# Performance work log

Hardware: AMD Instinct MI355X
Metric: run time of the kernel (lower is better)

Reference implementation:

```python
import jax, jax.numpy as jnp
import numpy as np

DIM = 1536
HEADS = 12
HD = DIM // HEADS           # 128
C = HD // 2                 # 64 rotary pairs per head
B = 1
F_, H_, W_ = 16, 16, 16
S = F_ * H_ * W_            # 4096
MAXPOS = 1024
EPS = 1e-6
SPLITS = (C - 2 * (C // 3), C // 3, C // 3)  # (22, 21, 21)


def setup_inputs() -> dict:
    key = jax.random.key(0)
    ks = jax.random.split(key, 8)
    std = 0.02
    x = jax.random.normal(ks[0], (B, S, DIM), jnp.float32)
    seq_lens = jnp.full((B,), S, dtype=jnp.int32)
    grid_sizes = jnp.tile(jnp.array([[F_, H_, W_]], jnp.int32), (B, 1))
    # rotary angle table: per split, theta_j = pos / 10000^(j/size)
    angs = []
    pos = jnp.arange(MAXPOS, dtype=jnp.float32)
    for sz in SPLITS:
        inv = 1.0 / (10000.0 ** (jnp.arange(sz, dtype=jnp.float32) / sz))
        angs.append(jnp.outer(pos, inv))
    freqs = jnp.concatenate(angs, axis=1)  # [MAXPOS, C]
    return {
        "x": x,
        "seq_lens": seq_lens,
        "grid_sizes": grid_sizes,
        "freqs": freqs,
        "wq": jax.random.normal(ks[1], (DIM, DIM), jnp.float32) * std,
        "bq": jnp.zeros((DIM,), jnp.float32),
        "wk": jax.random.normal(ks[2], (DIM, DIM), jnp.float32) * std,
        "bk": jnp.zeros((DIM,), jnp.float32),
        "wv": jax.random.normal(ks[3], (DIM, DIM), jnp.float32) * std,
        "bv": jnp.zeros((DIM,), jnp.float32),
        "wo": jax.random.normal(ks[4], (DIM, DIM), jnp.float32) * std,
        "bo": jnp.zeros((DIM,), jnp.float32),
        "gq": jnp.ones((DIM,), jnp.float32),
        "gk": jnp.ones((DIM,), jnp.float32),
    }


def _rms_norm(x, g):
    # x * rsqrt(mean(x^2) + eps) * g  (WanRMSNorm)
    var = jnp.mean(jnp.square(x), axis=-1, keepdims=True)
    return x * jax.lax.rsqrt(var + EPS) * g


def _rope(x, freqs, f, h, w):
    # x: [b, s, n, hd]; freqs: [MAXPOS, C] angles; grid (f,h,w), s = f*h*w
    fa = freqs[:f, : SPLITS[0]]
    ha = freqs[:h, SPLITS[0] : SPLITS[0] + SPLITS[1]]
    wa = freqs[:w, SPLITS[0] + SPLITS[1] :]
    ang = jnp.concatenate(
        [
            jnp.broadcast_to(fa[:, None, None, :], (f, h, w, SPLITS[0])),
            jnp.broadcast_to(ha[None, :, None, :], (f, h, w, SPLITS[1])),
            jnp.broadcast_to(wa[None, None, :, :], (f, h, w, SPLITS[2])),
        ],
        axis=-1,
    ).reshape(f * h * w, 1, C)  # [s, 1, C] broadcasts over heads
    cos, sin = jnp.cos(ang), jnp.sin(ang)
    xr = x[..., 0::2]  # real parts of complex pairs
    xi = x[..., 1::2]  # imag parts
    out_r = xr * cos - xi * sin
    out_i = xr * sin + xi * cos
    return jnp.stack([out_r, out_i], axis=-1).reshape(x.shape)


def reference(x, seq_lens, grid_sizes, freqs, wq, bq, wk, bk, wv, bv, wo, bo, gq, gk):
    b, s = x.shape[:2]
    q = _rms_norm(x @ wq.T + bq, gq).reshape(b, s, HEADS, HD)
    k = _rms_norm(x @ wk.T + bk, gk).reshape(b, s, HEADS, HD)
    v = (x @ wv.T + bv).reshape(b, s, HEADS, HD)
    # all samples share the same grid (static for jit)
    q = _rope(q, freqs, F_, H_, W_)
    k = _rope(k, freqs, F_, H_, W_)
    scale = 1.0 / np.sqrt(HD)
    scores = jnp.einsum("bqnd,bknd->bnqk", q, k) * scale  # [b, n, s, s]
    k_pos = jnp.arange(s)
    mask = k_pos[None, None, None, :] < seq_lens[:, None, None, None]
    scores = scores + jnp.where(mask, 0.0, -1e9)
    attn = jax.nn.softmax(scores, axis=-1)
    out = jnp.einsum("bnqk,bknd->bqnd", attn, v).reshape(b, s, DIM)
    return out @ wo.T + bo
```

## Files before the change

kernel.cpp:

```cpp
#include <hip/hip_runtime.h>
#include <hip/hip_bf16.h>

#define DIM   1536
#define HEADS 12
#define HD    128
#define SEQ   4096
#define QSCALE 0.08838834764831845f
#define LOG2E 1.44269504088896f

typedef __attribute__((ext_vector_type(8))) short short8;
typedef __attribute__((ext_vector_type(4))) float f32x4;
typedef __attribute__((ext_vector_type(16))) float f32x16;

__device__ __forceinline__ unsigned short f2bf(float f) {
    __hip_bfloat16 h = __float2bfloat16(f);
    return *reinterpret_cast<unsigned short*>(&h);
}
__device__ __forceinline__ float bf2f(unsigned short u) {
    return __uint_as_float(((unsigned int)u) << 16);
}
__device__ __forceinline__ void async_cp16(void* lds, const void* g) {
    __builtin_amdgcn_global_load_lds(
        (const __attribute__((address_space(1))) unsigned int*)g,
        (__attribute__((address_space(3))) unsigned int*)lds, 16, 0, 0);
}

__global__ __launch_bounds__(256) void convert_bf16(
    const float* __restrict__ src, __hip_bfloat16* __restrict__ dst, int n8)
{
    const int i = blockIdx.x * 256 + threadIdx.x;
    if (i >= n8) return;
    const float4 a = *reinterpret_cast<const float4*>(src + (size_t)i * 8);
    const float4 b = *reinterpret_cast<const float4*>(src + (size_t)i * 8 + 4);
    uint4 o;
    o.x = (unsigned int)f2bf(a.x) | ((unsigned int)f2bf(a.y) << 16);
    o.y = (unsigned int)f2bf(a.z) | ((unsigned int)f2bf(a.w) << 16);
    o.z = (unsigned int)f2bf(b.x) | ((unsigned int)f2bf(b.y) << 16);
    o.w = (unsigned int)f2bf(b.z) | ((unsigned int)f2bf(b.w) << 16);
    *reinterpret_cast<uint4*>(dst + (size_t)i * 8) = o;
}

__global__ __launch_bounds__(256) void convert_all(
    const float* __restrict__ x,  const float* __restrict__ wq,
    const float* __restrict__ wk, const float* __restrict__ wv,
    __hip_bfloat16* __restrict__ xb,  __hip_bfloat16* __restrict__ wqb,
    __hip_bfloat16* __restrict__ wkb, __hip_bfloat16* __restrict__ wvb)
{
    const int i = blockIdx.x * 256 + threadIdx.x;
    const float* src;
    __hip_bfloat16* dst;
    int off;
    if (i < 786432)            { src = x;  dst = xb;  off = i; }
    else if (i < 1081344)      { src = wq; dst = wqb; off = i - 786432; }
    else if (i < 1376256)      { src = wk; dst = wkb; off = i - 1081344; }
    else                       { src = wv; dst = wvb; off = i - 1376256; }
    const float4 a = *reinterpret_cast<const float4*>(src + (size_t)off * 8);
    const float4 b = *reinterpret_cast<const float4*>(src + (size_t)off * 8 + 4);
    uint4 o;
    o.x = (unsigned int)f2bf(a.x) | ((unsigned int)f2bf(a.y) << 16);
    o.y = (unsigned int)f2bf(a.z) | ((unsigned int)f2bf(a.w) << 16);
    o.z = (unsigned int)f2bf(b.x) | ((unsigned int)f2bf(b.y) << 16);
    o.w = (unsigned int)f2bf(b.z) | ((unsigned int)f2bf(b.w) << 16);
    *reinterpret_cast<uint4*>(dst + (size_t)off * 8) = o;
}

__global__ __launch_bounds__(256) void gemm_qkv(
    const __hip_bfloat16* __restrict__ xb,
    const __hip_bfloat16* __restrict__ wqb, const float* __restrict__ bq,
    const __hip_bfloat16* __restrict__ wkb, const float* __restrict__ bk,
    const __hip_bfloat16* __restrict__ wvb, const float* __restrict__ bv,
    __hip_bfloat16* __restrict__ yq, __hip_bfloat16* __restrict__ yk,
    __hip_bfloat16* __restrict__ vrow)
{
    __shared__ __align__(16) short As[128][32];
    __shared__ __align__(16) short Bs[128][32];
    const int z  = blockIdx.z;
    const __hip_bfloat16* W = (z == 0) ? wqb : (z == 1) ? wkb : wvb;
    const float* bias = (z == 0) ? bq : (z == 1) ? bk : bv;
    __hip_bfloat16* outp = (z == 0) ? yq : (z == 1) ? yk : vrow;
    const int bm0 = blockIdx.x * 128;
    const int bn0 = blockIdx.y * 128;
    const int tid  = threadIdx.x;
    const int lane = tid & 63;
    const int wid  = tid >> 6;
    const int wm = (wid >> 1) * 64;
    const int wn = (wid & 1)  * 64;
    const int fr = lane & 15;
    const int fc = (lane >> 4) * 8;
    const int srow = tid >> 2;
    const int scol = (tid & 3) * 8;

    f32x4 acc[4][4] = {};

    for (int kt = 0; kt < DIM; kt += 32) {
        #pragma unroll
        for (int i = 0; i < 2; i++) {
            async_cp16(&As[i * 64 + (wid << 4)][0],
                       xb + (size_t)(bm0 + i * 64 + srow) * DIM + kt + scol);
            async_cp16(&Bs[i * 64 + (wid << 4)][0],
                       W + (size_t)(bn0 + i * 64 + srow) * DIM + kt + scol);
        }
        __syncthreads();
        short8 af[4], bf8[4];
        #pragma unroll
        for (int m = 0; m < 4; m++) af[m]  = *reinterpret_cast<const short8*>(&As[wm + m * 16 + fr][fc]);
        #pragma unroll
        for (int n = 0; n < 4; n++) bf8[n] = *reinterpret_cast<const short8*>(&Bs[wn + n * 16 + fr][fc]);
        #pragma unroll
        for (int m = 0; m < 4; m++)
            #pragma unroll
            for (int n = 0; n < 4; n++)
                acc[m][n] = __builtin_amdgcn_mfma_f32_16x16x32_bf16(af[m], bf8[n], acc[m][n], 0, 0, 0);
        __syncthreads();
    }

    const int crow0 = bm0 + wm + (lane >> 4) * 4;
    const int ccol0 = bn0 + wn + fr;
    #pragma unroll
    for (int n = 0; n < 4; n++) {
        const int col = ccol0 + n * 16;
        const float bb = bias[col];
        #pragma unroll
        for (int m = 0; m < 4; m++)
            #pragma unroll
            for (int r = 0; r < 4; r++)
                outp[(size_t)(crow0 + m * 16 + r) * DIM + col] =
                    __float2bfloat16(acc[m][n][r] + bb);
    }
}

__global__ __launch_bounds__(256) void norm_rope_transpose(
    __hip_bfloat16* __restrict__ yq, __hip_bfloat16* __restrict__ yk,
    const float* __restrict__ gq, const float* __restrict__ gk,
    const float* __restrict__ freqs,
    const __hip_bfloat16* __restrict__ vrow, __hip_bfloat16* __restrict__ vT)
{
    __shared__ float red[4];
    __shared__ __align__(16) short tile[64][72];
    const int b = blockIdx.x;
    const int t = threadIdx.x;

    if (b < 8192) {
        const int s = b >> 1;
        const int z = b & 1;
        __hip_bfloat16* y = z ? yk : yq;
        const float* g = z ? gk : gq;

        float xr[3], xi[3];
        float ss = 0.f;
        #pragma unroll
        for (int i = 0; i < 3; i++) {
            const int p = t + i * 256;
            const unsigned int uu = *reinterpret_cast<const unsigned int*>(&y[(size_t)s * DIM + 2 * p]);
            xr[i] = bf2f((unsigned short)(uu & 0xffffu));
            xi[i] = bf2f((unsigned short)(uu >> 16));
            ss += xr[i] * xr[i] + xi[i] * xi[i];
        }
        #pragma unroll
        for (int m = 1; m < 64; m <<= 1) ss += __shfl_xor(ss, m, 64);
        if ((t & 63) == 0) red[t >> 6] = ss;
        __syncthreads();
        const float sum = red[0] + red[1] + red[2] + red[3];
        const float rs = rsqrtf(sum * (1.0f / DIM) + 1e-6f);
        const int f = s >> 8, hh = (s >> 4) & 15, ww = s & 15;
        const float osc = z ? 1.0f : QSCALE;
        #pragma unroll
        for (int i = 0; i < 3; i++) {
            const int p = t + i * 256;
            const int cc = p & 63;
            const int pos = (cc < 22) ? f : (cc < 43) ? hh : ww;
            const float ang = freqs[pos * 64 + cc];
            float sn, cs;
            sincosf(ang, &sn, &cs);
            const float a = xr[i] * rs * g[2 * p];
            const float bb = xi[i] * rs * g[2 * p + 1];
            const unsigned int pk = (unsigned int)f2bf((a * cs - bb * sn) * osc)
                                  | ((unsigned int)f2bf((a * sn + bb * cs) * osc) << 16);
            *reinterpret_cast<unsigned int*>(&y[(size_t)s * DIM + 2 * p]) = pk;
        }
    } else {
        const int tb = b - 8192;
        const int s0 = (tb & 63) * 64;
        const int c0 = (tb >> 6) * 64;
        #pragma unroll
        for (int i = 0; i < 2; i++) {
            const int ch = t + i * 256;
            const int r = ch >> 3, cc = (ch & 7) * 8;
            *reinterpret_cast<int4*>(&tile[r][cc]) =
                *reinterpret_cast<const int4*>(&vrow[(size_t)(s0 + r) * DIM + c0 + cc]);
        }
        __syncthreads();
        #pragma unroll
        for (int i = 0; i < 2; i++) {
            const int ch = t + i * 256;
            const int c = ch & 63, sc = (ch >> 6) * 8;
            unsigned int w0 = (unsigned short)tile[sc + 0][c] | ((unsigned int)(unsigned short)tile[sc + 1][c] << 16);
            unsigned int w1 = (unsigned short)tile[sc + 2][c] | ((unsigned int)(unsigned short)tile[sc + 3][c] << 16);
            unsigned int w2 = (unsigned short)tile[sc + 4][c] | ((unsigned int)(unsigned short)tile[sc + 5][c] << 16);
            unsigned int w3 = (unsigned short)tile[sc + 6][c] | ((unsigned int)(unsigned short)tile[sc + 7][c] << 16);
            int4 val;
            val.x = (int)w0; val.y = (int)w1; val.z = (int)w2; val.w = (int)w3;
            *reinterpret_cast<int4*>(&vT[(size_t)(c0 + c) * SEQ + s0 + sc]) = val;
        }
    }
}

__global__ __launch_bounds__(256, 2) void flash_attn(
    const __hip_bfloat16* __restrict__ qb,
    const __hip_bfloat16* __restrict__ kb,
    const __hip_bfloat16* __restrict__ vT,
    const int* __restrict__ seq_lens,
    __hip_bfloat16* __restrict__ attno)
{
    __shared__ __align__(16) short Ks[2][64][128];
    __shared__ __align__(16) short Vs[3][128][64];
    const int qt = blockIdx.x;
    const int h  = blockIdx.y;
    const int tid = threadIdx.x;
    const int lane = tid & 63;
    const int w = tid >> 6;
    const int q5 = lane & 31;
    const int hi = lane >> 5;
    const int seqlen = seq_lens[0];
    const int swz = (lane & 7) << 4;
    const int NT = SEQ / 64;

    short8 qf[8];
    const int qrow = qt * 128 + w * 32 + q5;
    #pragma unroll
    for (int s = 0; s < 8; s++)
        qf[s] = *reinterpret_cast<const short8*>(&qb[(size_t)qrow * DIM + h * HD + s * 16 + hi * 8]);

    f32x16 oacc[4] = {};
    float m = -1e30f, l = 0.f;
    unsigned int WpG[4][4];

    const int kROW = w * 4 + (lane >> 4);
    const int kCOL = ((lane & 15) ^ (kROW & 7)) * 8;
    const int vROW = w * 8 + (lane >> 3);
    const int vCOL = (((lane & 7) ^ (vROW & 7))) * 8;

    auto stageK = [&](int tile, int slot) {
        #pragma unroll
        for (int i = 0; i < 4; i++)
            async_cp16(&Ks[slot][i * 16 + w * 4][0],
                       kb + (size_t)(tile * 64 + i * 16 + kROW) * DIM + h * HD + kCOL);
    };
    auto stageV = [&](int tile, int slot) {
        #pragma unroll
        for (int i = 0; i < 4; i++)
            async_cp16(&Vs[slot][i * 32 + vROW][0],
                       vT + ((size_t)h * HD + i * 32 + vROW) * SEQ + tile * 64 + vCOL);
    };
    auto pv = [&](int slot) {
        const char* Vp = (const char*)&Vs[slot][0][0];
        __builtin_amdgcn_s_setprio(1);
        #pragma unroll
        for (int ks = 0; ks < 4; ks++) {
            int4 pwv;
            pwv.x = (int)WpG[ks][0];
            pwv.y = (int)WpG[ks][1];
            pwv.z = (int)WpG[ks][2];
            pwv.w = (int)WpG[ks][3];
            const short8 pf = __builtin_bit_cast(short8, pwv);
            #pragma unroll
            for (int cb = 0; cb < 4; cb++) {
                short8 vf = *reinterpret_cast<const short8*>(
                    Vp + (cb * 32 + q5) * 128 + ((ks * 32 + hi * 16) ^ swz));
                oacc[cb] = __builtin_amdgcn_mfma_f32_32x32x16_bf16(vf, pf, oacc[cb], 0, 0, 0);
            }
        }
        __builtin_amdgcn_s_setprio(0);
    };
    auto softmax_pack = [&](int tt, f32x16* S) {
        const int kbase = tt * 64;
        float v[32];
        if (kbase + 64 <= seqlen) {
            #pragma unroll
            for (int kbk = 0; kbk < 2; kbk++)
                #pragma unroll
                for (int r = 0; r < 16; r++) v[kbk * 16 + r] = S[kbk][r];
        } else {
            #pragma unroll
            for (int kbk = 0; kbk < 2; kbk++)
                #pragma unroll
                for (int r = 0; r < 16; r++) {
                    const int key = kbase + kbk * 32 + (r & 3) + 8 * (r >> 2) + 4 * hi;
                    const float sv = (key < seqlen) ? S[kbk][r] : -1e30f;
                    S[kbk][r] = sv;
                    v[kbk * 16 + r] = sv;
                }
        }
        #pragma unroll
        for (int st = 16; st >= 1; st >>= 1)
            #pragma unroll
            for (int i = 0; i < st; i++) v[i] = fmaxf(v[i], v[i + st]);
        float tmax = fmaxf(v[0], __shfl_xor(v[0], 32, 64));

        if (!__all(tmax <= m + 8.0f)) {
            const float mn = fmaxf(m, tmax);
            const float alpha = exp2f((m - mn) * LOG2E);
            m = mn;
            l *= alpha;
            #pragma unroll
            for (int cb = 0; cb < 4; cb++)
                #pragma unroll
                for (int r = 0; r < 16; r++) oacc[cb][r] *= alpha;
        }
        const float nmL = -m * LOG2E;
        #pragma unroll
        for (int kbk = 0; kbk < 2; kbk++)
            #pragma unroll
            for (int r = 0; r < 16; r++) {
                const float p = exp2f(fmaf(S[kbk][r], LOG2E, nmL));
                S[kbk][r] = p;
                v[kbk * 16 + r] = p;
            }
        #pragma unroll
        for (int st = 16; st >= 1; st >>= 1)
            #pragma unroll
            for (int i = 0; i < st; i++) v[i] += v[i + st];
        l += v[0] + __shfl_xor(v[0], 32, 64);

        unsigned int Wl[2][4][2];
        #pragma unroll
        for (int kbk = 0; kbk < 2; kbk++)
            #pragma unroll
            for (int tq = 0; tq < 4; tq++) {
                Wl[kbk][tq][0] = (unsigned int)f2bf(S[kbk][4 * tq + 0])
                               | ((unsigned int)f2bf(S[kbk][4 * tq + 1]) << 16);
                Wl[kbk][tq][1] = (unsigned int)f2bf(S[kbk][4 * tq + 2])
                               | ((unsigned int)f2bf(S[kbk][4 * tq + 3]) << 16);
            }
        #pragma unroll
        for (int ks = 0; ks < 4; ks++) {
            const int kbk = ks >> 1;
            const int te = (ks & 1) * 2, to = te + 1;
            const int a0 = (int)Wl[kbk][te][0], a1 = (int)Wl[kbk][te][1];
            const int b0 = (int)Wl[kbk][to][0], b1 = (int)Wl[kbk][to][1];
            const int xa0 = __shfl_xor(a0, 32, 64);
            const int xa1 = __shfl_xor(a1, 32, 64);
            const int xb0 = __shfl_xor(b0, 32, 64);
            const int xb1 = __shfl_xor(b1, 32, 64);
            WpG[ks][0] = (unsigned int)(hi ? xb0 : a0);
            WpG[ks][1] = (unsigned int)(hi ? xb1 : a1);
            WpG[ks][2] = (unsigned int)(hi ? b0  : xa0);
            WpG[ks][3] = (unsigned int)(hi ? b1  : xa1);
        }
    };
    auto qk = [&](int slot, f32x16* S) {
        const char* Kp = (const char*)&Ks[slot][0][0];
        __builtin_amdgcn_s_setprio(1);
        #pragma unroll
        for (int s = 0; s < 8; s++)
            #pragma unroll
            for (int kbk = 0; kbk < 2; kbk++) {
                short8 kf = *reinterpret_cast<const short8*>(
                    Kp + (kbk * 32 + q5) * 256 + ((s * 32 + hi * 16) ^ swz));
                S[kbk] = __builtin_amdgcn_mfma_f32_32x32x16_bf16(kf, qf[s], S[kbk], 0, 0, 0);
            }
        __builtin_amdgcn_s_setprio(0);
    };

    stageK(0, 0); stageV(0, 0);
    __syncthreads();
    stageK(1, 1); stageV(1, 1);
    {
        f32x16 sacc[2] = {};
        qk(0, sacc);
        softmax_pack(0, sacc);
    }

    int vprev = 0, vnext = 2;
    for (int t = 1; t < NT; t++) {
        __syncthreads();
        if (t + 1 < NT) {
            stageK(t + 1, (t + 1) & 1);
            stageV(t + 1, vnext);
        }
        f32x16 sacc[2] = {};
        qk(t & 1, sacc);
        pv(vprev);
        softmax_pack(t, sacc);
        vprev = (vprev == 2) ? 0 : vprev + 1;
        vnext = (vnext == 2) ? 0 : vnext + 1;
    }

    pv(vprev);

    const float inv_l = 1.f / l;
    const size_t obase = (size_t)qrow * DIM + h * HD;
    #pragma unroll
    for (int cb = 0; cb < 4; cb++) {
        #pragma unroll
        for (int tq = 0; tq < 4; tq++) {
            uint2 pko;
            pko.x = (unsigned int)f2bf(oacc[cb][4 * tq + 0] * inv_l)
                  | ((unsigned int)f2bf(oacc[cb][4 * tq + 1] * inv_l) << 16);
            pko.y = (unsigned int)f2bf(oacc[cb][4 * tq + 2] * inv_l)
                  | ((unsigned int)f2bf(oacc[cb][4 * tq + 3] * inv_l) << 16);
            *reinterpret_cast<uint2*>(&attno[obase + cb * 32 + 8 * tq + 4 * hi]) = pko;
        }
    }
}

__global__ __launch_bounds__(256) void gemm_out(
    const __hip_bfloat16* __restrict__ A,
    const __hip_bfloat16* __restrict__ W,
    const float* __restrict__ bias,
    float* __restrict__ outp)
{
    __shared__ __align__(16) short As[128][32];
    __shared__ __align__(16) short Bs[128][32];
    const int bm0 = blockIdx.x * 128;
    const int bn0 = blockIdx.y * 128;
    const int tid = threadIdx.x;
    const int lane = tid & 63;
    const int wid = tid >> 6;
    const int wm = (wid >> 1) * 64;
    const int wn = (wid & 1) * 64;
    const int fr = lane & 15;
    const int fc = (lane >> 4) * 8;
    const int srow = tid >> 2;
    const int scol = (tid & 3) * 8;

    f32x4 acc[4][4] = {};

    for (int kt = 0; kt < DIM; kt += 32) {
        #pragma unroll
        for (int i = 0; i < 2; i++) {
            async_cp16(&As[i * 64 + (wid << 4)][0],
                       A + (size_t)(bm0 + i * 64 + srow) * DIM + kt + scol);
            async_cp16(&Bs[i * 64 + (wid << 4)][0],
                       W + (size_t)(bn0 + i * 64 + srow) * DIM + kt + scol);
        }
        __syncthreads();
        short8 af[4], bf8[4];
        #pragma unroll
        for (int m = 0; m < 4; m++) af[m]  = *reinterpret_cast<const short8*>(&As[wm + m * 16 + fr][fc]);
        #pragma unroll
        for (int n = 0; n < 4; n++) bf8[n] = *reinterpret_cast<const short8*>(&Bs[wn + n * 16 + fr][fc]);
        #pragma unroll
        for (int m = 0; m < 4; m++)
            #pragma unroll
            for (int n = 0; n < 4; n++)
                acc[m][n] = __builtin_amdgcn_mfma_f32_16x16x32_bf16(af[m], bf8[n], acc[m][n], 0, 0, 0);
        __syncthreads();
    }

    const int crow0 = bm0 + wm + (lane >> 4) * 4;
    const int ccol0 = bn0 + wn + fr;
    #pragma unroll
    for (int n = 0; n < 4; n++) {
        const int col = ccol0 + n * 16;
        const float bb = bias[col];
        #pragma unroll
        for (int m = 0; m < 4; m++)
            #pragma unroll
            for (int r = 0; r < 4; r++)
                outp[(size_t)(crow0 + m * 16 + r) * DIM + col] = acc[m][n][r] + bb;
    }
}

extern "C" void kernel_launch(void* const* d_in, const int* in_sizes, int n_in,
                              void* d_out, int out_size, void* d_ws, size_t ws_size,
                              hipStream_t stream)
{
    const float* x        = (const float*)d_in[0];
    const int*   seq_lens = (const int*)d_in[1];
    const float* freqs    = (const float*)d_in[3];
    const float* wq = (const float*)d_in[4];
    const float* bq = (const float*)d_in[5];
    const float* wk = (const float*)d_in[6];
    const float* bk = (const float*)d_in[7];
    const float* wv = (const float*)d_in[8];
    const float* bv = (const float*)d_in[9];
    const float* wo = (const float*)d_in[10];
    const float* bo = (const float*)d_in[11];
    const float* gq = (const float*)d_in[12];
    const float* gk = (const float*)d_in[13];
    float* out = (float*)d_out;

    char* ws = (char*)d_ws;
    __hip_bfloat16* yq    = (__hip_bfloat16*)(ws);
    __hip_bfloat16* yk    = (__hip_bfloat16*)(ws + 12582912);
    __hip_bfloat16* vrow  = (__hip_bfloat16*)(ws + 25165824);
    __hip_bfloat16* vT    = (__hip_bfloat16*)(ws + 37748736);
    __hip_bfloat16* attno = (__hip_bfloat16*)(ws + 25165824);
    __hip_bfloat16* xb    = (__hip_bfloat16*)(ws + 37748736);
    __hip_bfloat16* wob   = (__hip_bfloat16*)(ws);
    __hip_bfloat16* wqb   = (__hip_bfloat16*)d_out;
    __hip_bfloat16* wkb   = wqb + 2359296;
    __hip_bfloat16* wvb   = wkb + 2359296;

    dim3 blk(256);
    convert_all        <<<dim3(6528), blk, 0, stream>>>(x, wq, wk, wv, xb, wqb, wkb, wvb);
    gemm_qkv           <<<dim3(32, 12, 3), blk, 0, stream>>>(xb, wqb, bq, wkb, bk, wvb, bv, yq, yk, vrow);
    norm_rope_transpose<<<dim3(9728), blk, 0, stream>>>(yq, yk, gq, gk, freqs, vrow, vT);
    flash_attn         <<<dim3(32, 12), blk, 0, stream>>>(yq, yk, vT, seq_lens, attno);
    convert_bf16       <<<dim3(1152), blk, 0, stream>>>(wo, wob, 294912);
    gemm_out           <<<dim3(32, 12), blk, 0, stream>>>(attno, wob, bo, out);
}
```

Before: 323.3 us.

## Process two 32-row query tiles per wave in flash attention with 128-thread blocks

Result: slower. 406.3 us (+25.7%).

```diff
diff --git a/kernel.cpp b/kernel.cpp
--- a/kernel.cpp
+++ b/kernel.cpp
@@ -205,7 +205,7 @@
     }
 }
 
-__global__ __launch_bounds__(256, 2) void flash_attn(
+__global__ __launch_bounds__(128, 1) void flash_attn(
     const __hip_bfloat16* __restrict__ qb,
     const __hip_bfloat16* __restrict__ kb,
     const __hip_bfloat16* __restrict__ vT,
@@ -225,71 +225,90 @@
     const int swz = (lane & 7) << 4;
     const int NT = SEQ / 64;
 
-    short8 qf[8];
-    const int qrow = qt * 128 + w * 32 + q5;
+    const int qrowA = qt * 128 + w * 64 + q5;
+    const int qrowB = qrowA + 32;
+    short8 qfA[8], qfB[8];
     #pragma unroll
-    for (int s = 0; s < 8; s++)
-        qf[s] = *reinterpret_cast<const short8*>(&qb[(size_t)qrow * DIM + h * HD + s * 16 + hi * 8]);
-
-    f32x16 oacc[4] = {};
-    float m = -1e30f, l = 0.f;
-    unsigned int WpG[4][4];
-
-    const int kROW = w * 4 + (lane >> 4);
-    const int kCOL = ((lane & 15) ^ (kROW & 7)) * 8;
-    const int vROW = w * 8 + (lane >> 3);
-    const int vCOL = (((lane & 7) ^ (vROW & 7))) * 8;
+    for (int s = 0; s < 8; s++) {
+        qfA[s] = *reinterpret_cast<const short8*>(&qb[(size_t)qrowA * DIM + h * HD + s * 16 + hi * 8]);
+        qfB[s] = *reinterpret_cast<const short8*>(&qb[(size_t)qrowB * DIM + h * HD + s * 16 + hi * 8]);
+    }
+
+    f32x16 oaccA[4] = {}, oaccB[4] = {};
+    float mA = -1e30f, lA = 0.f, mB = -1e30f, lB = 0.f;
+    unsigned int WpGA[4][4], WpGB[4][4];
+
+    const int kROW0 = w * 4 + (lane >> 4);
+    const int kCOL  = ((lane & 15) ^ kROW0) * 8;
+    const int vROW0 = w * 8 + (lane >> 3);
+    const int vCOL  = ((lane & 7) ^ (vROW0 & 7)) * 8;
 
     auto stageK = [&](int tile, int slot) {
         #pragma unroll
-        for (int i = 0; i < 4; i++)
-            async_cp16(&Ks[slot][i * 16 + w * 4][0],
-                       kb + (size_t)(tile * 64 + i * 16 + kROW) * DIM + h * HD + kCOL);
+        for (int i = 0; i < 8; i++)
+            async_cp16(&Ks[slot][i * 8 + w * 4][0],
+                       kb + (size_t)(tile * 64 + i * 8 + kROW0) * DIM + h * HD + kCOL);
     };
     auto stageV = [&](int tile, int slot) {
         #pragma unroll
-        for (int i = 0; i < 4; i++)
-            async_cp16(&Vs[slot][i * 32 + vROW][0],
-                       vT + ((size_t)h * HD + i * 32 + vROW) * SEQ + tile * 64 + vCOL);
+        for (int i = 0; i < 8; i++)
+            async_cp16(&Vs[slot][i * 16 + vROW0][0],
+                       vT + ((size_t)h * HD + i * 16 + vROW0) * SEQ + tile * 64 + vCOL);
+    };
+    auto qk = [&](int slot, f32x16* SA, f32x16* SB) {
+        const char* Kp = (const char*)&Ks[slot][0][0];
+        __builtin_amdgcn_s_setprio(1);
+        #pragma unroll
+        for (int s = 0; s < 8; s++) {
+            #pragma unroll
+            for (int kbk = 0; kbk < 2; kbk++) {
+                short8 kf = *reinterpret_cast<const short8*>(
+                    Kp + (kbk * 32 + q5) * 256 + ((s * 32 + hi * 16) ^ swz));
+                SA[kbk] = __builtin_amdgcn_mfma_f32_32x32x16_bf16(kf, qfA[s], SA[kbk], 0, 0, 0);
+                SB[kbk] = __builtin_amdgcn_mfma_f32_32x32x16_bf16(kf, qfB[s], SB[kbk], 0, 0, 0);
+            }
+        }
+        __builtin_amdgcn_s_setprio(0);
     };
     auto pv = [&](int slot) {
         const char* Vp = (const char*)&Vs[slot][0][0];
         __builtin_amdgcn_s_setprio(1);
         #pragma unroll
         for (int ks = 0; ks < 4; ks++) {
-            int4 pwv;
-            pwv.x = (int)WpG[ks][0];
-            pwv.y = (int)WpG[ks][1];
-            pwv.z = (int)WpG[ks][2];
-            pwv.w = (int)WpG[ks][3];
-            const short8 pf = __builtin_bit_cast(short8, pwv);
+            int4 pa, pb;
+            pa.x = (int)WpGA[ks][0]; pa.y = (int)WpGA[ks][1];
+            pa.z = (int)WpGA[ks][2]; pa.w = (int)WpGA[ks][3];
+            pb.x = (int)WpGB[ks][0]; pb.y = (int)WpGB[ks][1];
+            pb.z = (int)WpGB[ks][2]; pb.w = (int)WpGB[ks][3];
+            const short8 pfA = __builtin_bit_cast(short8, pa);
+            const short8 pfB = __builtin_bit_cast(short8, pb);
             #pragma unroll
             for (int cb = 0; cb < 4; cb++) {
                 short8 vf = *reinterpret_cast<const short8*>(
                     Vp + (cb * 32 + q5) * 128 + ((ks * 32 + hi * 16) ^ swz));
-                oacc[cb] = __builtin_amdgcn_mfma_f32_32x32x16_bf16(vf, pf, oacc[cb], 0, 0, 0);
+                oaccA[cb] = __builtin_amdgcn_mfma_f32_32x32x16_bf16(vf, pfA, oaccA[cb], 0, 0, 0);
+                oaccB[cb] = __builtin_amdgcn_mfma_f32_32x32x16_bf16(vf, pfB, oaccB[cb], 0, 0, 0);
             }
         }
         __builtin_amdgcn_s_setprio(0);
     };
-    auto softmax_pack = [&](int tt, f32x16* S) {
+    auto softmax_pack = [&](int tt, f32x16& S0, f32x16& S1,
+                            float& mm, float& ll, f32x16* oc,
+                            unsigned int (*WG)[4]) {
         const int kbase = tt * 64;
         float v[32];
         if (kbase + 64 <= seqlen) {
             #pragma unroll
-            for (int kbk = 0; kbk < 2; kbk++)
-                #pragma unroll
-                for (int r = 0; r < 16; r++) v[kbk * 16 + r] = S[kbk][r];
+            for (int r = 0; r < 16; r++) { v[r] = S0[r]; v[16 + r] = S1[r]; }
         } else {
             #pragma unroll
-            for (int kbk = 0; kbk < 2; kbk++)
-                #pragma unroll
-                for (int r = 0; r < 16; r++) {
-                    const int key = kbase + kbk * 32 + (r & 3) + 8 * (r >> 2) + 4 * hi;
-                    const float sv = (key < seqlen) ? S[kbk][r] : -1e30f;
-                    S[kbk][r] = sv;
-                    v[kbk * 16 + r] = sv;
-                }
+            for (int r = 0; r < 16; r++) {
+                const int key0 = kbase + (r & 3) + 8 * (r >> 2) + 4 * hi;
+                const float s0 = (key0 < seqlen) ? S0[r] : -1e30f;
+                const float s1 = (key0 + 32 < seqlen) ? S1[r] : -1e30f;
+                S0[r] = s0; S1[r] = s1;
+                v[r] = s0; v[16 + r] = s1;
+            }
         }
         #pragma unroll
         for (int st = 16; st >= 1; st >>= 1)
@@ -297,41 +316,38 @@
             for (int i = 0; i < st; i++) v[i] = fmaxf(v[i], v[i + st]);
         float tmax = fmaxf(v[0], __shfl_xor(v[0], 32, 64));
 
-        if (!__all(tmax <= m + 8.0f)) {
-            const float mn = fmaxf(m, tmax);
-            const float alpha = exp2f((m - mn) * LOG2E);
-            m = mn;
-            l *= alpha;
+        if (!__all(tmax <= mm + 8.0f)) {
+            const float mn = fmaxf(mm, tmax);
+            const float alpha = exp2f((mm - mn) * LOG2E);
+            mm = mn;
+            ll *= alpha;
             #pragma unroll
             for (int cb = 0; cb < 4; cb++)
                 #pragma unroll
-                for (int r = 0; r < 16; r++) oacc[cb][r] *= alpha;
-        }
-        const float nmL = -m * LOG2E;
-        #pragma unroll
-        for (int kbk = 0; kbk < 2; kbk++)
-            #pragma unroll
-            for (int r = 0; r < 16; r++) {
-                const float p = exp2f(fmaf(S[kbk][r], LOG2E, nmL));
-                S[kbk][r] = p;
-                v[kbk * 16 + r] = p;
-            }
+                for (int r = 0; r < 16; r++) oc[cb][r] *= alpha;
+        }
+        const float nmL = -mm * LOG2E;
+        #pragma unroll
+        for (int r = 0; r < 16; r++) {
+            const float p0 = exp2f(fmaf(S0[r], LOG2E, nmL));
+            const float p1 = exp2f(fmaf(S1[r], LOG2E, nmL));
+            S0[r] = p0; S1[r] = p1;
+            v[r] = p0; v[16 + r] = p1;
+        }
         #pragma unroll
         for (int st = 16; st >= 1; st >>= 1)
             #pragma unroll
             for (int i = 0; i < st; i++) v[i] += v[i + st];
-        l += v[0] + __shfl_xor(v[0], 32, 64);
+        ll += v[0] + __shfl_xor(v[0], 32, 64);
 
         unsigned int Wl[2][4][2];
         #pragma unroll
-        for (int kbk = 0; kbk < 2; kbk++)
-            #pragma unroll
-            for (int tq = 0; tq < 4; tq++) {
-                Wl[kbk][tq][0] = (unsigned int)f2bf(S[kbk][4 * tq + 0])
-                               | ((unsigned int)f2bf(S[kbk][4 * tq + 1]) << 16);
-                Wl[kbk][tq][1] = (unsigned int)f2bf(S[kbk][4 * tq + 2])
-                               | ((unsigned int)f2bf(S[kbk][4 * tq + 3]) << 16);
-            }
+        for (int tq = 0; tq < 4; tq++) {
+            Wl[0][tq][0] = (unsigned int)f2bf(S0[4 * tq + 0]) | ((unsigned int)f2bf(S0[4 * tq + 1]) << 16);
+            Wl[0][tq][1] = (unsigned int)f2bf(S0[4 * tq + 2]) | ((unsigned int)f2bf(S0[4 * tq + 3]) << 16);
+            Wl[1][tq][0] = (unsigned int)f2bf(S1[4 * tq + 0]) | ((unsigned int)f2bf(S1[4 * tq + 1]) << 16);
+            Wl[1][tq][1] = (unsigned int)f2bf(S1[4 * tq + 2]) | ((unsigned int)f2bf(S1[4 * tq + 3]) << 16);
+        }
         #pragma unroll
         for (int ks = 0; ks < 4; ks++) {
             const int kbk = ks >> 1;
@@ -342,33 +358,21 @@
             const int xa1 = __shfl_xor(a1, 32, 64);
             const int xb0 = __shfl_xor(b0, 32, 64);
             const int xb1 = __shfl_xor(b1, 32, 64);
-            WpG[ks][0] = (unsigned int)(hi ? xb0 : a0);
-            WpG[ks][1] = (unsigned int)(hi ? xb1 : a1);
-            WpG[ks][2] = (unsigned int)(hi ? b0  : xa0);
-            WpG[ks][3] = (unsigned int)(hi ? b1  : xa1);
-        }
-    };
-    auto qk = [&](int slot, f32x16* S) {
-        const char* Kp = (const char*)&Ks[slot][0][0];
-        __builtin_amdgcn_s_setprio(1);
-        #pragma unroll
-        for (int s = 0; s < 8; s++)
-            #pragma unroll
-            for (int kbk = 0; kbk < 2; kbk++) {
-                short8 kf = *reinterpret_cast<const short8*>(
-                    Kp + (kbk * 32 + q5) * 256 + ((s * 32 + hi * 16) ^ swz));
-                S[kbk] = __builtin_amdgcn_mfma_f32_32x32x16_bf16(kf, qf[s], S[kbk], 0, 0, 0);
-            }
-        __builtin_amdgcn_s_setprio(0);
+            WG[ks][0] = (unsigned int)(hi ? xb0 : a0);
+            WG[ks][1] = (unsigned int)(hi ? xb1 : a1);
+            WG[ks][2] = (unsigned int)(hi ? b0  : xa0);
+            WG[ks][3] = (unsigned int)(hi ? b1  : xa1);
+        }
     };
 
     stageK(0, 0); stageV(0, 0);
     __syncthreads();
     stageK(1, 1); stageV(1, 1);
     {
-        f32x16 sacc[2] = {};
-        qk(0, sacc);
-        softmax_pack(0, sacc);
+        f32x16 SA[2] = {}, SB[2] = {};
+        qk(0, SA, SB);
+        softmax_pack(0, SA[0], SA[1], mA, lA, oaccA, WpGA);
+        softmax_pack(0, SB[0], SB[1], mB, lB, oaccB, WpGB);
     }
 
     int vprev = 0, vnext = 2;
@@ -378,28 +382,35 @@
             stageK(t + 1, (t + 1) & 1);
             stageV(t + 1, vnext);
         }
-        f32x16 sacc[2] = {};
-        qk(t & 1, sacc);
+        f32x16 SA[2] = {}, SB[2] = {};
+        qk(t & 1, SA, SB);
         pv(vprev);
-        softmax_pack(t, sacc);
+        softmax_pack(t, SA[0], SA[1], mA, lA, oaccA, WpGA);
+        softmax_pack(t, SB[0], SB[1], mB, lB, oaccB, WpGB);
         vprev = (vprev == 2) ? 0 : vprev + 1;
         vnext = (vnext == 2) ? 0 : vnext + 1;
     }
 
     pv(vprev);
 
-    const float inv_l = 1.f / l;
-    const size_t obase = (size_t)qrow * DIM + h * HD;
+    const float invA = 1.f / lA, invB = 1.f / lB;
+    const size_t obA = (size_t)qrowA * DIM + h * HD;
+    const size_t obB = (size_t)qrowB * DIM + h * HD;
     #pragma unroll
     for (int cb = 0; cb < 4; cb++) {
         #pragma unroll
         for (int tq = 0; tq < 4; tq++) {
-            uint2 pko;
-            pko.x = (unsigned int)f2bf(oacc[cb][4 * tq + 0] * inv_l)
-                  | ((unsigned int)f2bf(oacc[cb][4 * tq + 1] * inv_l) << 16);
-            pko.y = (unsigned int)f2bf(oacc[cb][4 * tq + 2] * inv_l)
-                  | ((unsigned int)f2bf(oacc[cb][4 * tq + 3] * inv_l) << 16);
-            *reinterpret_cast<uint2*>(&attno[obase + cb * 32 + 8 * tq + 4 * hi]) = pko;
+            uint2 pa, pb;
+            pa.x = (unsigned int)f2bf(oaccA[cb][4 * tq + 0] * invA)
+                 | ((unsigned int)f2bf(oaccA[cb][4 * tq + 1] * invA) << 16);
+            pa.y = (unsigned int)f2bf(oaccA[cb][4 * tq + 2] * invA)
+                 | ((unsigned int)f2bf(oaccA[cb][4 * tq + 3] * invA) << 16);
+            pb.x = (unsigned int)f2bf(oaccB[cb][4 * tq + 0] * invB)
+                 | ((unsigned int)f2bf(oaccB[cb][4 * tq + 1] * invB) << 16);
+            pb.y = (unsigned int)f2bf(oaccB[cb][4 * tq + 2] * invB)
+                 | ((unsigned int)f2bf(oaccB[cb][4 * tq + 3] * invB) << 16);
+            *reinterpret_cast<uint2*>(&attno[obA + cb * 32 + 8 * tq + 4 * hi]) = pa;
+            *reinterpret_cast<uint2*>(&attno[obB + cb * 32 + 8 * tq + 4 * hi]) = pb;
         }
     }
 }
@@ -497,7 +508,7 @@
     convert_all        <<<dim3(6528), blk, 0, stream>>>(x, wq, wk, wv, xb, wqb, wkb, wvb);
     gemm_qkv           <<<dim3(32, 12, 3), blk, 0, stream>>>(xb, wqb, bq, wkb, bk, wvb, bv, yq, yk, vrow);
     norm_rope_transpose<<<dim3(9728), blk, 0, stream>>>(yq, yk, gq, gk, freqs, vrow, vT);
-    flash_attn         <<<dim3(32, 12), blk, 0, stream>>>(yq, yk, vT, seq_lens, attno);
+    flash_attn         <<<dim3(32, 12), dim3(128), 0, stream>>>(yq, yk, vT, seq_lens, attno);
     convert_bf16       <<<dim3(1152), blk, 0, stream>>>(wo, wob, 294912);
     gemm_out           <<<dim3(32, 12), blk, 0, stream>>>(attno, wob, bo, out);
 }
```
